# Kernel optimization log

Hardware: AMD Instinct MI355X
Metric: run time of the kernel (lower is better)

Reference implementation:

```python
import jax, jax.numpy as jnp
import numpy as np

B, S, D, H, F = 8, 1024, 1024, 16, 4096
DH = D // H  # 64
EPS = 1e-12


def _layer_norm(x, g, b):
    mu = jnp.mean(x, axis=-1, keepdims=True)
    var = jnp.mean(jnp.square(x - mu), axis=-1, keepdims=True)
    return (x - mu) / jnp.sqrt(var + EPS) * g + b


def setup_inputs() -> dict:
    key = jax.random.key(0)
    ks = jax.random.split(key, 16)
    sd = 0.02
    inp = {
        "x": jax.random.normal(ks[0], (B, S, D), dtype=jnp.float32),
        "attn_mask": jnp.ones((B, S), dtype=jnp.int32),
        # attention projections (torch Linear: W is [out, in])
        "Wq": jax.random.normal(ks[1], (D, D), dtype=jnp.float32) * sd,
        "bq": jnp.zeros((D,), dtype=jnp.float32),
        "Wk": jax.random.normal(ks[2], (D, D), dtype=jnp.float32) * sd,
        "bk": jnp.zeros((D,), dtype=jnp.float32),
        "Wv": jax.random.normal(ks[3], (D, D), dtype=jnp.float32) * sd,
        "bv": jnp.zeros((D,), dtype=jnp.float32),
        "Wo": jax.random.normal(ks[4], (D, D), dtype=jnp.float32) * sd,
        "bo": jnp.zeros((D,), dtype=jnp.float32),
        # sa_layer_norm
        "ln1_g": jnp.ones((D,), dtype=jnp.float32),
        "ln1_b": jnp.zeros((D,), dtype=jnp.float32),
        # FFN
        "W1": jax.random.normal(ks[5], (F, D), dtype=jnp.float32) * sd,
        "b1": jnp.zeros((F,), dtype=jnp.float32),
        "W2": jax.random.normal(ks[6], (D, F), dtype=jnp.float32) * sd,
        "b2": jnp.zeros((D,), dtype=jnp.float32),
        # output_layer_norm
        "ln2_g": jnp.ones((D,), dtype=jnp.float32),
        "ln2_b": jnp.zeros((D,), dtype=jnp.float32),
    }
    return inp


def reference(x, attn_mask, Wq, bq, Wk, bk, Wv, bv, Wo, bo,
              ln1_g, ln1_b, W1, b1, W2, b2, ln2_g, ln2_b):
    b, s, d = x.shape

    def proj_heads(inp, W, bias):
        y = jnp.einsum('bsd,ed->bse', inp, W) + bias  # torch Linear: x @ W.T + b
        return y.reshape(b, s, H, DH).transpose(0, 2, 1, 3)  # (b, h, s, dh)

    q = proj_heads(x, Wq, bq) / jnp.sqrt(jnp.float32(DH))
    k = proj_heads(x, Wk, bk)
    v = proj_heads(x, Wv, bv)

    scores = jnp.einsum('bhqe,bhke->bhqk', q, k)  # (b, h, s, s)
    pad = (attn_mask == 0)[:, None, None, :]      # (b, 1, 1, s)
    scores = jnp.where(pad, -jnp.inf, scores)
    weights = jax.nn.softmax(scores, axis=-1)

    ctx = jnp.einsum('bhqk,bhke->bhqe', weights, v)
    ctx = ctx.transpose(0, 2, 1, 3).reshape(b, s, d)
    sa_out = jnp.einsum('bsd,ed->bse', ctx, Wo) + bo

    h = _layer_norm(sa_out + x, ln1_g, ln1_b)

    ff = jnp.einsum('bsd,fd->bsf', h, W1) + b1
    ff = jax.nn.gelu(ff, approximate=False)
    ff = jnp.einsum('bsf,df->bsd', ff, W2) + b2

    out = _layer_norm(ff + h, ln2_g, ln2_b)
    return out
```

## Files before the change

### kernel.cpp

```cpp
#include <hip/hip_runtime.h>
#include <math.h>

typedef __attribute__((ext_vector_type(8))) short short8;
typedef __attribute__((ext_vector_type(4))) float f32x4;

__device__ __forceinline__ unsigned short f2bf(float f) {
  unsigned int u = __float_as_uint(f);
  u += 0x7fffu + ((u >> 16) & 1u);
  return (unsigned short)(u >> 16);
}

__device__ __forceinline__ float gelu_f(float v) {
  float xa = fabsf(v) * 0.70710678118f;
  float t = __builtin_amdgcn_rcpf(1.f + 0.3275911f * xa);
  float p = t * (0.254829592f +
            t * (-0.284496736f +
            t * (1.421413741f +
            t * (-1.453152027f + t * 1.061405429f))));
  float erfa = 1.f - p * __expf(-xa * xa);
  return 0.5f * v * (1.f + copysignf(erfa, v));
}

__device__ __forceinline__ void gll16(const unsigned short* g, unsigned short* l) {
  __builtin_amdgcn_global_load_lds(
      (const __attribute__((address_space(1))) unsigned int*)(uintptr_t)g,
      (__attribute__((address_space(3))) unsigned int*)(uintptr_t)l, 16, 0, 0);
}

__global__ __launch_bounds__(256) void cvt_all(
    const float* __restrict__ Wq, const float* __restrict__ Wk,
    const float* __restrict__ Wv, const float* __restrict__ Wo,
    const float* __restrict__ W1, const float* __restrict__ W2,
    const float* __restrict__ x, unsigned short* __restrict__ ws) {
  const int bi = blockIdx.x;
  const float* in;
  unsigned short* out;
  int i;
  if (bi < 4096) {
    const int m = bi >> 10;
    in = (m == 0) ? Wq : (m == 1) ? Wk : (m == 2) ? Wv : Wo;
    out = ws + (size_t)m * (1u << 20);
    i = (bi & 1023) * 256 + threadIdx.x;
  } else if (bi < 8192) {
    in = W1; out = ws + (4u << 20); i = (bi - 4096) * 256 + threadIdx.x;
  } else if (bi < 12288) {
    in = W2; out = ws + (8u << 20); i = (bi - 8192) * 256 + threadIdx.x;
  } else {
    in = x; out = ws + (12u << 20); i = (bi - 12288) * 256 + threadIdx.x;
  }
  float4 f = reinterpret_cast<const float4*>(in)[i];
  ushort4 o;
  o.x = f2bf(f.x); o.y = f2bf(f.y); o.z = f2bf(f.z); o.w = f2bf(f.w);
  reinterpret_cast<ushort4*>(out)[i] = o;
}

#define MFMA_Q(mh, nh)                                                        \
  {                                                                           \
    __builtin_amdgcn_s_setprio(1);                                            \
    _Pragma("unroll") for (int i = 0; i < 4; ++i) {                           \
      _Pragma("unroll") for (int jj = 0; jj < NREP / 2; ++jj) {               \
        const int j = (nh) * (NREP / 2) + jj;                                 \
        if constexpr (SWAP) {                                                 \
          acc[(mh) * 4 + i][j] = __builtin_amdgcn_mfma_f32_16x16x32_bf16(     \
              bf[j][0], af[i][0], acc[(mh) * 4 + i][j], 0, 0, 0);             \
          acc[(mh) * 4 + i][j] = __builtin_amdgcn_mfma_f32_16x16x32_bf16(     \
              bf[j][1], af[i][1], acc[(mh) * 4 + i][j], 0, 0, 0);             \
        } else {                                                              \
          acc[(mh) * 4 + i][j] = __builtin_amdgcn_mfma_f32_16x16x32_bf16(     \
              af[i][0], bf[j][0], acc[(mh) * 4 + i][j], 0, 0, 0);             \
          acc[(mh) * 4 + i][j] = __builtin_amdgcn_mfma_f32_16x16x32_bf16(     \
              af[i][1], bf[j][1], acc[(mh) * 4 + i][j], 0, 0, 0);             \
        }                                                                     \
      }                                                                       \
    }                                                                         \
    __builtin_amdgcn_s_setprio(0);                                            \
  }

#define READ_A(mh)                                                            \
  _Pragma("unroll") for (int i = 0; i < 4; ++i) {                             \
    af[i][0] = *reinterpret_cast<const short8*>(                              \
        &Asc[abase + ((mh) * 64 + i * 16) * 64 + s0]);                        \
    af[i][1] = *reinterpret_cast<const short8*>(                              \
        &Asc[abase + ((mh) * 64 + i * 16) * 64 + s1]);                        \
  }

#define READ_B(nh)                                                            \
  _Pragma("unroll") for (int jj = 0; jj < NREP / 2; ++jj) {                   \
    const int j = (nh) * (NREP / 2) + jj;                                     \
    bf[j][0] = *reinterpret_cast<const short8*>(                              \
        &Bsc[bbase + (j * 16) * 64 + s0]);                                    \
    bf[j][1] = *reinterpret_cast<const short8*>(                              \
        &Bsc[bbase + (j * 16) * 64 + s1]);                                    \
  }

#define LGKM0                                                                 \
  asm volatile("s_waitcnt lgkmcnt(0)" ::: "memory");                          \
  __builtin_amdgcn_sched_barrier(0)

#define MEMFENCE asm volatile("" ::: "memory")
#define BAR __builtin_amdgcn_s_barrier()

template <int EPI, int BN, bool SWAP>
__global__ __launch_bounds__(512, 2) void gemm_big(
    const unsigned short* __restrict__ A, const unsigned short* __restrict__ B,
    const float* __restrict__ bias, const float* __restrict__ bias_k,
    int K, int N, const float* __restrict__ resid,
    unsigned short* __restrict__ outb, float* __restrict__ outf) {
  constexpr int WN = BN / 4;
  constexpr int NREP = WN / 16;
  constexpr int BGRP = BN / 64;
  __shared__ __align__(16) unsigned short As[2][256 * 64];
  __shared__ __align__(16) unsigned short Bs[2][BN * 64];

  const int t = threadIdx.x;
  const int lane = t & 63, wv = t >> 6;
  const int wm = wv >> 2, wn = wv & 3;
  const int l15 = lane & 15, quad = lane >> 4;

  const int gx = gridDim.x;
  const int nwg = gx * gridDim.y;
  int lin = blockIdx.y * gx + blockIdx.x;
  lin = (lin & 7) * (nwg >> 3) + (lin >> 3);
  const int gxs = 31 - __clz(gx);
  const int tn = (lin & (gx - 1)) * BN;
  const int tm = (lin >> gxs) * 256;

  const int srow = lane >> 3;
  const int scol = ((lane & 7) ^ srow) << 3;
  const unsigned short* pA[4];
  const unsigned short* pB[BGRP];
#pragma unroll
  for (int g = 0; g < 4; ++g)
    pA[g] = &A[(size_t)(tm + g * 64 + wv * 8 + srow) * K + scol];
#pragma unroll
  for (int g = 0; g < BGRP; ++g)
    pB[g] = &B[(size_t)(tn + g * 64 + wv * 8 + srow) * K + scol];

  const int abase = (wm * 128 + l15) * 64;
  const int bbase = (wn * WN + l15) * 64;
  const int s0 = ((quad ^ (l15 & 7)) << 3);
  const int s1 = (((quad + 4) ^ (l15 & 7)) << 3);

  const f32x4 zero = {0.f, 0.f, 0.f, 0.f};
  f32x4 acc[8][NREP];
#pragma unroll
  for (int i = 0; i < 8; ++i)
#pragma unroll
    for (int j = 0; j < NREP; ++j) acc[i][j] = zero;
  short8 af[4][2], bf[NREP][2];

  gll16(pA[0], &As[0][(0 * 64 + wv * 8) * 64]);
  gll16(pA[2], &As[0][(2 * 64 + wv * 8) * 64]);
#pragma unroll
  for (int g = 0; g < BGRP; ++g) gll16(pB[g], &Bs[0][(g * 64 + wv * 8) * 64]);
  gll16(pA[1], &As[0][(1 * 64 + wv * 8) * 64]); pA[1] += 64;
  gll16(pA[3], &As[0][(3 * 64 + wv * 8) * 64]); pA[3] += 64;
  pA[0] += 64;
  gll16(pA[0], &As[1][(0 * 64 + wv * 8) * 64]); pA[0] += 64;
  pA[2] += 64;
  gll16(pA[2], &As[1][(2 * 64 + wv * 8) * 64]); pA[2] += 64;
#pragma unroll
  for (int g = 0; g < BGRP; ++g) {
    pB[g] += 64;
    gll16(pB[g], &Bs[1][(g * 64 + wv * 8) * 64]);
    pB[g] += 64;
  }
  if constexpr (BGRP == 4) asm volatile("s_waitcnt vmcnt(6)" ::: "memory");
  else asm volatile("s_waitcnt vmcnt(4)" ::: "memory");
  BAR;
  MEMFENCE;

  const int NT = K >> 6;
  for (int tt = 0; tt < NT; ++tt) {
    const unsigned short* Asc = As[tt & 1];
    const unsigned short* Bsc = Bs[tt & 1];
    unsigned short* Asw = As[tt & 1];
    unsigned short* Bsw = Bs[tt & 1];
    unsigned short* Asn = As[(tt + 1) & 1];

    if (tt + 1 < NT) {
      gll16(pA[1], &Asn[(1 * 64 + wv * 8) * 64]); pA[1] += 64;
      gll16(pA[3], &Asn[(3 * 64 + wv * 8) * 64]); pA[3] += 64;
    }
    READ_A(0);
    READ_B(0);
    __builtin_amdgcn_sched_barrier(0);
    READ_B(1);
    MEMFENCE; BAR;
    if constexpr (NREP == 4) asm volatile("s_waitcnt lgkmcnt(4)" ::: "memory");
    else asm volatile("s_waitcnt lgkmcnt(2)" ::: "memory");
    __builtin_amdgcn_sched_barrier(0);
    MFMA_Q(0, 0);
    LGKM0;
    MFMA_Q(0, 1);
    MEMFENCE; BAR;

    if (tt + 2 < NT) {
      gll16(pA[0], &Asw[(0 * 64 + wv * 8) * 64]); pA[0] += 64;
      gll16(pA[2], &Asw[(2 * 64 + wv * 8) * 64]); pA[2] += 64;
#pragma unroll
      for (int g = 0; g < BGRP; ++g) {
        gll16(pB[g], &Bsw[(g * 64 + wv * 8) * 64]);
        pB[g] += 64;
      }
    }
    READ_A(1);
    MEMFENCE; BAR;
    LGKM0;
    MFMA_Q(1, 0);
    MFMA_Q(1, 1);
    if (tt + 2 < NT) {
      if constexpr (BGRP == 4) asm volatile("s_waitcnt vmcnt(6)" ::: "memory");
      else asm volatile("s_waitcnt vmcnt(4)" ::: "memory");
    } else {
      asm volatile("s_waitcnt vmcnt(0)" ::: "memory");
    }
    MEMFENCE; BAR;
  }

  if constexpr (!SWAP) {
    const int rb2 = tm + wm * 128 + (quad << 2);
    const int cb2 = tn + wn * WN + l15;
#pragma unroll
    for (int i = 0; i < 8; ++i) {
      const int row0 = rb2 + i * 16;
#pragma unroll
      for (int j = 0; j < NREP; ++j) {
        const int col = cb2 + j * 16;
        const float bcol = bias[col];
        const int h = col >> 6, dh = col & 63;
        const int b = row0 >> 10, s0r = row0 & 1023;
        ushort4 pk;
        pk.x = f2bf(acc[i][j][0] + bcol);
        pk.y = f2bf(acc[i][j][1] + bcol);
        pk.z = f2bf(acc[i][j][2] + bcol);
        pk.w = f2bf(acc[i][j][3] + bcol);
        *reinterpret_cast<ushort4*>(
            &outb[(((size_t)((b << 4) + h)) << 16) + (dh << 10) + s0r]) = pk;
      }
    }
  } else {
    const int rb = tm + wm * 128 + l15;
    const int cb = tn + wn * WN + (quad << 2);
#pragma unroll
    for (int i = 0; i < 8; ++i) {
      const int row = rb + i * 16;
#pragma unroll
      for (int j = 0; j < NREP; ++j) {
        const int col0 = cb + j * 16;
        if constexpr (EPI == 5) {
          const int chunk = col0 >> 10;
          const int colc = col0 & 1023;
          const float4 b4 = *reinterpret_cast<const float4*>(
              &(chunk == 0 ? bias : bias_k)[colc]);
          const float sc = (chunk == 0) ? 0.125f : 1.f;
          const int h = colc >> 6, dh = colc & 63;
          const int b = row >> 10, s = row & 1023;
          ushort4 pk;
          pk.x = f2bf((acc[i][j][0] + b4.x) * sc);
          pk.y = f2bf((acc[i][j][1] + b4.y) * sc);
          pk.z = f2bf((acc[i][j][2] + b4.z) * sc);
          pk.w = f2bf((acc[i][j][3] + b4.w) * sc);
          *reinterpret_cast<ushort4*>(
              &outb[((size_t)chunk << 23) + (((size_t)((b << 4) + h)) << 16) +
                    (s << 6) + dh]) = pk;
        } else if constexpr (EPI == 2) {
          const float4 b4 = *reinterpret_cast<const float4*>(&bias[col0]);
          ushort4 pk;
          pk.x = f2bf(gelu_f(acc[i][j][0] + b4.x));
          pk.y = f2bf(gelu_f(acc[i][j][1] + b4.y));
          pk.z = f2bf(gelu_f(acc[i][j][2] + b4.z));
          pk.w = f2bf(gelu_f(acc[i][j][3] + b4.w));
          *reinterpret_cast<ushort4*>(&outb[(size_t)row * (size_t)N + col0]) = pk;
        } else {
          const float4 b4 = *reinterpret_cast<const float4*>(&bias[col0]);
          const size_t idx = (size_t)row * (size_t)N + col0;
          const float4 r4 = *reinterpret_cast<const float4*>(&resid[idx]);
          float4 o4;
          o4.x = acc[i][j][0] + b4.x + r4.x;
          o4.y = acc[i][j][1] + b4.y + r4.y;
          o4.z = acc[i][j][2] + b4.z + r4.z;
          o4.w = acc[i][j][3] + b4.w + r4.w;
          *reinterpret_cast<float4*>(&outf[idx]) = o4;
        }
      }
    }
  }
}
#undef MFMA_Q
#undef READ_A
#undef READ_B
#undef LGKM0
#undef MEMFENCE
#undef BAR

__global__ __launch_bounds__(256) void attn_kernel(
    const unsigned short* __restrict__ Q, const unsigned short* __restrict__ Kc,
    const unsigned short* __restrict__ Vg, const int* __restrict__ mask,
    unsigned short* __restrict__ ctx) {
  __shared__ __align__(16) unsigned short Ks[2][64 * 64];
  __shared__ __align__(16) unsigned short Vs[2][64 * 64];
  __shared__ __align__(16) unsigned short Ps[4][16 * 72];
  __shared__ float maskf[1024];
  const int t = threadIdx.x;
  const int bh = blockIdx.x;
  const int qt = blockIdx.y;
  const int b = bh >> 4, h = bh & 15;
  const int lane = t & 63, wv = t >> 6, l15 = lane & 15, quad = lane >> 4;
  const int lr = lane >> 3;
  const int cs = (lane & 7) ^ lr;
  const unsigned short* Qp = Q + ((size_t)bh << 16);
  const unsigned short* Kp = Kc + ((size_t)bh << 16);
  const unsigned short* Vp = Vg + ((size_t)bh << 16);
  const int seg0 = wv * 2, seg1 = wv * 2 + 1;
  const int r0 = seg0 * 8 + lr, r1 = seg1 * 8 + lr;

  for (int i = t; i < 1024; i += 256)
    maskf[i] = mask[b * 1024 + i] ? -8.f : -INFINITY;

  short8 qf[2][2];
#pragma unroll
  for (int g = 0; g < 2; ++g)
#pragma unroll
    for (int hh = 0; hh < 2; ++hh)
      qf[g][hh] = *reinterpret_cast<const short8*>(
          &Qp[(size_t)(qt * 128 + wv * 32 + g * 16 + l15) * 64 + hh * 32 + quad * 8]);

  gll16(&Kp[r0 * 64 + cs * 8], &Ks[0][seg0 * 512]);
  gll16(&Kp[r1 * 64 + cs * 8], &Ks[0][seg1 * 512]);
  gll16(&Vp[r0 * 1024 + cs * 8], &Vs[0][seg0 * 512]);
  gll16(&Vp[r1 * 1024 + cs * 8], &Vs[0][seg1 * 512]);

  const int sw0 = ((quad ^ (l15 & 7)) << 3);
  const int sw1 = (((quad + 4) ^ (l15 & 7)) << 3);
  const f32x4 zero = {0.f, 0.f, 0.f, 0.f};
  float ps[2][4];
  f32x4 o[2][4];
#pragma unroll
  for (int g = 0; g < 2; ++g)
#pragma unroll
    for (int j = 0; j < 4; ++j) { o[g][j] = zero; ps[g][j] = 0.f; }

  unsigned short* Pw = Ps[wv];
  for (int kt = 0; kt < 16; ++kt) {
    __syncthreads();
    const int cur = kt & 1;
    if (kt < 15) {
      const int nb = cur ^ 1;
      gll16(&Kp[((kt + 1) * 64 + r0) * 64 + cs * 8], &Ks[nb][seg0 * 512]);
      gll16(&Kp[((kt + 1) * 64 + r1) * 64 + cs * 8], &Ks[nb][seg1 * 512]);
      gll16(&Vp[r0 * 1024 + (kt + 1) * 64 + cs * 8], &Vs[nb][seg0 * 512]);
      gll16(&Vp[r1 * 1024 + (kt + 1) * 64 + cs * 8], &Vs[nb][seg1 * 512]);
    }
    float madd[4];
    short8 kf[4][2];
#pragma unroll
    for (int nt = 0; nt < 4; ++nt) {
      const int row = (nt * 16 + l15) * 64;
      kf[nt][0] = *reinterpret_cast<const short8*>(&Ks[cur][row + sw0]);
      kf[nt][1] = *reinterpret_cast<const short8*>(&Ks[cur][row + sw1]);
      madd[nt] = maskf[kt * 64 + nt * 16 + l15];
    }
#pragma unroll
    for (int g = 0; g < 2; ++g) {
      f32x4 s4[4];
#pragma unroll
      for (int nt = 0; nt < 4; ++nt) {
        s4[nt] = __builtin_amdgcn_mfma_f32_16x16x32_bf16(qf[g][0], kf[nt][0], zero, 0, 0, 0);
        s4[nt] = __builtin_amdgcn_mfma_f32_16x16x32_bf16(qf[g][1], kf[nt][1], s4[nt], 0, 0, 0);
      }
#pragma unroll
      for (int nt = 0; nt < 4; ++nt) {
#pragma unroll
        for (int r = 0; r < 4; ++r) {
          float p = __expf(s4[nt][r] + madd[nt]);
          ps[g][r] += p;
          Pw[(quad * 4 + r) * 72 + nt * 16 + l15] = f2bf(p);
        }
      }
      short8 pf0 = *reinterpret_cast<const short8*>(&Pw[l15 * 72 + quad * 8]);
      short8 pf1 = *reinterpret_cast<const short8*>(&Pw[l15 * 72 + 32 + quad * 8]);
#pragma unroll
      for (int nt = 0; nt < 4; ++nt) {
        const int row = (nt * 16 + l15) * 64;
        short8 vf0 = *reinterpret_cast<const short8*>(&Vs[cur][row + sw0]);
        short8 vf1 = *reinterpret_cast<const short8*>(&Vs[cur][row + sw1]);
        o[g][nt] = __builtin_amdgcn_mfma_f32_16x16x32_bf16(pf0, vf0, o[g][nt], 0, 0, 0);
        o[g][nt] = __builtin_amdgcn_mfma_f32_16x16x32_bf16(pf1, vf1, o[g][nt], 0, 0, 0);
      }
    }
  }

#pragma unroll
  for (int g = 0; g < 2; ++g)
#pragma unroll
    for (int r = 0; r < 4; ++r) {
      float v = ps[g][r];
#pragma unroll
      for (int off = 8; off >= 1; off >>= 1) v += __shfl_xor(v, off, 64);
      const float inv = 1.f / v;
      const int srow = qt * 128 + wv * 32 + g * 16 + quad * 4 + r;
#pragma unroll
      for (int nt = 0; nt < 4; ++nt) {
        const int dh = nt * 16 + l15;
        ctx[((size_t)b << 20) + ((size_t)srow << 10) + (h << 6) + dh] =
            f2bf(o[g][nt][r] * inv);
      }
    }
}

__global__ __launch_bounds__(256) void ln_kernel(float* __restrict__ y,
                                                 const float* __restrict__ g,
                                                 const float* __restrict__ be,
                                                 unsigned short* __restrict__ hb) {
  __shared__ float sm[8];
  const int t = threadIdx.x;
  const size_t row = blockIdx.x;
  float* yr = y + (row << 10);
  float v[4];
#pragma unroll
  for (int i = 0; i < 4; ++i) v[i] = yr[t + (i << 8)];
  float s = v[0] + v[1] + v[2] + v[3];
#pragma unroll
  for (int off = 32; off >= 1; off >>= 1) s += __shfl_xor(s, off, 64);
  if ((t & 63) == 0) sm[t >> 6] = s;
  __syncthreads();
  float mu = (sm[0] + sm[1] + sm[2] + sm[3]) * (1.f / 1024.f);
  float q = 0.f;
#pragma unroll
  for (int i = 0; i < 4; ++i) { float d = v[i] - mu; q += d * d; }
#pragma unroll
  for (int off = 32; off >= 1; off >>= 1) q += __shfl_xor(q, off, 64);
  if ((t & 63) == 0) sm[4 + (t >> 6)] = q;
  __syncthreads();
  float var = (sm[4] + sm[5] + sm[6] + sm[7]) * (1.f / 1024.f);
  float rs = rsqrtf(var + 1e-12f);
#pragma unroll
  for (int i = 0; i < 4; ++i) {
    int c = t + (i << 8);
    float o = (v[i] - mu) * rs * g[c] + be[c];
    yr[c] = o;
    if (hb) hb[(row << 10) + c] = f2bf(o);
  }
}

extern "C" void kernel_launch(void* const* d_in, const int* in_sizes, int n_in,
                              void* d_out, int out_size, void* d_ws, size_t ws_size,
                              hipStream_t stream) {
  const float* x   = (const float*)d_in[0];
  const int*   msk = (const int*)d_in[1];
  const float* Wq  = (const float*)d_in[2];
  const float* bq  = (const float*)d_in[3];
  const float* Wk  = (const float*)d_in[4];
  const float* bk  = (const float*)d_in[5];
  const float* Wv  = (const float*)d_in[6];
  const float* bv  = (const float*)d_in[7];
  const float* Wo  = (const float*)d_in[8];
  const float* bo  = (const float*)d_in[9];
  const float* g1  = (const float*)d_in[10];
  const float* be1 = (const float*)d_in[11];
  const float* W1  = (const float*)d_in[12];
  const float* b1  = (const float*)d_in[13];
  const float* W2  = (const float*)d_in[14];
  const float* b2  = (const float*)d_in[15];
  const float* g2  = (const float*)d_in[16];
  const float* be2 = (const float*)d_in[17];
  float* out = (float*)d_out;

  unsigned short* Wqb = (unsigned short*)d_ws;
  unsigned short* Wvb = Wqb + (2u << 20);
  unsigned short* Wob = Wvb + (1u << 20);
  unsigned short* W1b = Wob + (1u << 20);
  unsigned short* W2b = W1b + (4u << 20);
  unsigned short* xb  = W2b + (4u << 20);
  unsigned short* qb  = xb + (8u << 20);
  unsigned short* vb  = qb + (16u << 20);
  unsigned short* ctx = xb;
  unsigned short* ffb = xb;
  float* y1 = (float*)(qb + (24u << 20));
  unsigned short* hb = (unsigned short*)(y1 + (8u << 20));

  dim3 blk(256), blk5(512);
  cvt_all<<<dim3(20480), blk, 0, stream>>>(Wq, Wk, Wv, Wo, W1, W2, x, (unsigned short*)d_ws);
  gemm_big<5, 256, true><<<dim3(8, 32), blk5, 0, stream>>>(xb, Wqb, bq, bk, 1024, 2048,
                                                           nullptr, qb, nullptr);
  gemm_big<4, 128, false><<<dim3(8, 32), blk5, 0, stream>>>(xb, Wvb, bv, nullptr, 1024, 1024,
                                                            nullptr, vb, nullptr);
  attn_kernel<<<dim3(128, 8), blk, 0, stream>>>(qb, qb + (8u << 20), vb, msk, ctx);
  gemm_big<1, 128, true><<<dim3(8, 32), blk5, 0, stream>>>(ctx, Wob, bo, nullptr, 1024, 1024,
                                                           x, nullptr, y1);
  ln_kernel<<<dim3(8192), blk, 0, stream>>>(y1, g1, be1, hb);
  gemm_big<2, 256, true><<<dim3(16, 32), blk5, 0, stream>>>(hb, W1b, b1, nullptr, 1024, 4096,
                                                            nullptr, ffb, nullptr);
  gemm_big<1, 128, true><<<dim3(8, 32), blk5, 0, stream>>>(ffb, W2b, b2, nullptr, 4096, 1024,
                                                           y1, nullptr, out);
  ln_kernel<<<dim3(8192), blk, 0, stream>>>(out, g2, be2, nullptr);
}
```

Before: 496.9 us.

## Restructure GEMM main loop to one barrier per K-tile with register double-buffering

The big GEMM kernel's K loop is rewritten. It now prefetches the whole next A/B tile into the other LDS buffer at the start of each iteration and synchronises once at the end with vmcnt(0) plus a barrier. The old scheme used staggered half-tile loads and four barriers per iteration. A-fragment LDS reads are split into two alternating register sets so reads of the next 32-row slice overlap MFMAs on the current one. This cuts barrier count and scheduling stalls, but each prefetch now has only one tile of compute to hide behind, where the old scheme had deeper staggered overlap.

Measured after the change: 473.1 us. 4.8% less time.

```diff
diff --git a/kernel.cpp b/kernel.cpp
--- a/kernel.cpp
+++ b/kernel.cpp
@@ -54,47 +54,49 @@
   reinterpret_cast<ushort4*>(out)[i] = o;
 }
 
-#define MFMA_Q(mh, nh)                                                        \
+#define MFMA_SUB(f0, SA)                                                      \
   {                                                                           \
     __builtin_amdgcn_s_setprio(1);                                            \
-    _Pragma("unroll") for (int i = 0; i < 4; ++i) {                           \
-      _Pragma("unroll") for (int jj = 0; jj < NREP / 2; ++jj) {               \
-        const int j = (nh) * (NREP / 2) + jj;                                 \
+    _Pragma("unroll") for (int fi = 0; fi < 2; ++fi) {                        \
+      _Pragma("unroll") for (int j = 0; j < NREP; ++j) {                      \
         if constexpr (SWAP) {                                                 \
-          acc[(mh) * 4 + i][j] = __builtin_amdgcn_mfma_f32_16x16x32_bf16(     \
-              bf[j][0], af[i][0], acc[(mh) * 4 + i][j], 0, 0, 0);             \
-          acc[(mh) * 4 + i][j] = __builtin_amdgcn_mfma_f32_16x16x32_bf16(     \
-              bf[j][1], af[i][1], acc[(mh) * 4 + i][j], 0, 0, 0);             \
+          acc[(f0) + fi][j] = __builtin_amdgcn_mfma_f32_16x16x32_bf16(        \
+              bf[j][0], SA[fi][0], acc[(f0) + fi][j], 0, 0, 0);               \
+          acc[(f0) + fi][j] = __builtin_amdgcn_mfma_f32_16x16x32_bf16(        \
+              bf[j][1], SA[fi][1], acc[(f0) + fi][j], 0, 0, 0);               \
         } else {                                                              \
-          acc[(mh) * 4 + i][j] = __builtin_amdgcn_mfma_f32_16x16x32_bf16(     \
-              af[i][0], bf[j][0], acc[(mh) * 4 + i][j], 0, 0, 0);             \
-          acc[(mh) * 4 + i][j] = __builtin_amdgcn_mfma_f32_16x16x32_bf16(     \
-              af[i][1], bf[j][1], acc[(mh) * 4 + i][j], 0, 0, 0);             \
+          acc[(f0) + fi][j] = __builtin_amdgcn_mfma_f32_16x16x32_bf16(        \
+              SA[fi][0], bf[j][0], acc[(f0) + fi][j], 0, 0, 0);               \
+          acc[(f0) + fi][j] = __builtin_amdgcn_mfma_f32_16x16x32_bf16(        \
+              SA[fi][1], bf[j][1], acc[(f0) + fi][j], 0, 0, 0);               \
         }                                                                     \
       }                                                                       \
     }                                                                         \
     __builtin_amdgcn_s_setprio(0);                                            \
   }
 
-#define READ_A(mh)                                                            \
-  _Pragma("unroll") for (int i = 0; i < 4; ++i) {                             \
-    af[i][0] = *reinterpret_cast<const short8*>(                              \
-        &Asc[abase + ((mh) * 64 + i * 16) * 64 + s0]);                        \
-    af[i][1] = *reinterpret_cast<const short8*>(                              \
-        &Asc[abase + ((mh) * 64 + i * 16) * 64 + s1]);                        \
-  }
-
-#define READ_B(nh)                                                            \
-  _Pragma("unroll") for (int jj = 0; jj < NREP / 2; ++jj) {                   \
-    const int j = (nh) * (NREP / 2) + jj;                                     \
+#define READ_AF(SET, f0)                                                      \
+  {                                                                           \
+    SET[0][0] = *reinterpret_cast<const short8*>(                             \
+        &Asc[abase + ((f0) * 16) * 64 + s0]);                                 \
+    SET[0][1] = *reinterpret_cast<const short8*>(                             \
+        &Asc[abase + ((f0) * 16) * 64 + s1]);                                 \
+    SET[1][0] = *reinterpret_cast<const short8*>(                             \
+        &Asc[abase + ((f0) * 16 + 16) * 64 + s0]);                            \
+    SET[1][1] = *reinterpret_cast<const short8*>(                             \
+        &Asc[abase + ((f0) * 16 + 16) * 64 + s1]);                            \
+  }
+
+#define READ_BF                                                               \
+  _Pragma("unroll") for (int j = 0; j < NREP; ++j) {                          \
     bf[j][0] = *reinterpret_cast<const short8*>(                              \
         &Bsc[bbase + (j * 16) * 64 + s0]);                                    \
     bf[j][1] = *reinterpret_cast<const short8*>(                              \
         &Bsc[bbase + (j * 16) * 64 + s1]);                                    \
   }
 
-#define LGKM0                                                                 \
-  asm volatile("s_waitcnt lgkmcnt(0)" ::: "memory");                          \
+#define LGKM(n)                                                               \
+  asm volatile("s_waitcnt lgkmcnt(" #n ")" ::: "memory");                     \
   __builtin_amdgcn_sched_barrier(0)
 
 #define MEMFENCE asm volatile("" ::: "memory")
@@ -147,26 +149,19 @@
   for (int i = 0; i < 8; ++i)
 #pragma unroll
     for (int j = 0; j < NREP; ++j) acc[i][j] = zero;
-  short8 af[4][2], bf[NREP][2];
-
-  gll16(pA[0], &As[0][(0 * 64 + wv * 8) * 64]);
-  gll16(pA[2], &As[0][(2 * 64 + wv * 8) * 64]);
-#pragma unroll
-  for (int g = 0; g < BGRP; ++g) gll16(pB[g], &Bs[0][(g * 64 + wv * 8) * 64]);
-  gll16(pA[1], &As[0][(1 * 64 + wv * 8) * 64]); pA[1] += 64;
-  gll16(pA[3], &As[0][(3 * 64 + wv * 8) * 64]); pA[3] += 64;
-  pA[0] += 64;
-  gll16(pA[0], &As[1][(0 * 64 + wv * 8) * 64]); pA[0] += 64;
-  pA[2] += 64;
-  gll16(pA[2], &As[1][(2 * 64 + wv * 8) * 64]); pA[2] += 64;
+  short8 afA[2][2], afB[2][2], bf[NREP][2];
+
+#pragma unroll
+  for (int g = 0; g < 4; ++g) {
+    gll16(pA[g], &As[0][(g * 64 + wv * 8) * 64]);
+    pA[g] += 64;
+  }
 #pragma unroll
   for (int g = 0; g < BGRP; ++g) {
+    gll16(pB[g], &Bs[0][(g * 64 + wv * 8) * 64]);
     pB[g] += 64;
-    gll16(pB[g], &Bs[1][(g * 64 + wv * 8) * 64]);
-    pB[g] += 64;
-  }
-  if constexpr (BGRP == 4) asm volatile("s_waitcnt vmcnt(6)" ::: "memory");
-  else asm volatile("s_waitcnt vmcnt(4)" ::: "memory");
+  }
+  asm volatile("s_waitcnt vmcnt(0)" ::: "memory");
   BAR;
   MEMFENCE;
 
@@ -174,48 +169,41 @@
   for (int tt = 0; tt < NT; ++tt) {
     const unsigned short* Asc = As[tt & 1];
     const unsigned short* Bsc = Bs[tt & 1];
-    unsigned short* Asw = As[tt & 1];
-    unsigned short* Bsw = Bs[tt & 1];
     unsigned short* Asn = As[(tt + 1) & 1];
+    unsigned short* Bsn = Bs[(tt + 1) & 1];
 
     if (tt + 1 < NT) {
-      gll16(pA[1], &Asn[(1 * 64 + wv * 8) * 64]); pA[1] += 64;
-      gll16(pA[3], &Asn[(3 * 64 + wv * 8) * 64]); pA[3] += 64;
-    }
-    READ_A(0);
-    READ_B(0);
-    __builtin_amdgcn_sched_barrier(0);
-    READ_B(1);
-    MEMFENCE; BAR;
-    if constexpr (NREP == 4) asm volatile("s_waitcnt lgkmcnt(4)" ::: "memory");
-    else asm volatile("s_waitcnt lgkmcnt(2)" ::: "memory");
-    __builtin_amdgcn_sched_barrier(0);
-    MFMA_Q(0, 0);
-    LGKM0;
-    MFMA_Q(0, 1);
-    MEMFENCE; BAR;
-
-    if (tt + 2 < NT) {
-      gll16(pA[0], &Asw[(0 * 64 + wv * 8) * 64]); pA[0] += 64;
-      gll16(pA[2], &Asw[(2 * 64 + wv * 8) * 64]); pA[2] += 64;
+#pragma unroll
+      for (int g = 0; g < 4; ++g) {
+        gll16(pA[g], &Asn[(g * 64 + wv * 8) * 64]);
+        pA[g] += 64;
+      }
 #pragma unroll
       for (int g = 0; g < BGRP; ++g) {
-        gll16(pB[g], &Bsw[(g * 64 + wv * 8) * 64]);
+        gll16(pB[g], &Bsn[(g * 64 + wv * 8) * 64]);
         pB[g] += 64;
       }
     }
-    READ_A(1);
-    MEMFENCE; BAR;
-    LGKM0;
-    MFMA_Q(1, 0);
-    MFMA_Q(1, 1);
-    if (tt + 2 < NT) {
-      if constexpr (BGRP == 4) asm volatile("s_waitcnt vmcnt(6)" ::: "memory");
-      else asm volatile("s_waitcnt vmcnt(4)" ::: "memory");
-    } else {
+
+    READ_BF;
+    READ_AF(afA, 0);
+    READ_AF(afB, 2);
+    LGKM(4);
+    MFMA_SUB(0, afA);
+    READ_AF(afA, 4);
+    LGKM(4);
+    MFMA_SUB(2, afB);
+    READ_AF(afB, 6);
+    LGKM(4);
+    MFMA_SUB(4, afA);
+    LGKM(0);
+    MFMA_SUB(6, afB);
+
+    if (tt + 1 < NT) {
       asm volatile("s_waitcnt vmcnt(0)" ::: "memory");
-    }
-    MEMFENCE; BAR;
+      BAR;
+      MEMFENCE;
+    }
   }
 
   if constexpr (!SWAP) {
@@ -287,10 +275,10 @@
     }
   }
 }
-#undef MFMA_Q
-#undef READ_A
-#undef READ_B
-#undef LGKM0
+#undef MFMA_SUB
+#undef READ_AF
+#undef READ_BF
+#undef LGKM
 #undef MEMFENCE
 #undef BAR
 
```
